# Optimization experiments

Measured on AMD Instinct MI355X. Metric: run time of the kernel, lower is better.

The kernel has to match this reference:

```python
import jax, jax.numpy as jnp
import numpy as np

B, N, C, H, W = 16, 10, 128, 48, 48

def setup_inputs() -> dict:
    key = jax.random.key(0)
    k0, k1 = jax.random.split(key, 2)
    x = jax.random.normal(k0, (B, N, C, H, W), dtype=jnp.float32)
    # trainable interpolation params, initialized to 0.5 as in the torch module
    pos_dec = jnp.full((N,), 0.5, dtype=jnp.float32)
    length_dec = jnp.full((N,), 0.5, dtype=jnp.float32)
    # 1x1 conv == channel-mixing matmul over N*C channels
    NC = N * C
    conv_w = jax.random.normal(k1, (NC, NC), dtype=jnp.float32) * (1.0 / np.sqrt(NC))
    conv_b = jnp.zeros((NC,), dtype=jnp.float32)
    return {"x": x, "pos_dec": pos_dec, "length_dec": length_dec,
            "conv_w": conv_w, "conv_b": conv_b}


def reference(x, pos_dec, length_dec, conv_w, conv_b):
    b, n, c, h, w = x.shape
    d = c * h * w
    q = x.reshape(b, n, d)          # proj_query (B,N,CHW)
    k = q                           # proj_key has the same flattened features
    # bi_interpolate with pos_int=i, length_int=1 reduces in closed form to:
    #   s0 = (1-pd)*K[i]   + pd*K[i+1]                      (key_short row)
    #   s1 = ld*((1-pd)*K[i+1] + pd*K[i+2])                 (zero-padded short mixed with key_long)
    # where indices wrap mod N (key was concatenated with itself).
    idx = jnp.arange(n)
    k1_ = k[:, (idx + 1) % n]       # (B,N,D)
    k2_ = k[:, (idx + 2) % n]
    pd = pos_dec[None, :, None]
    ld = length_dec[None, :, None]
    s0 = (1.0 - pd) * k + pd * k1_
    s1 = ld * ((1.0 - pd) * k1_ + pd * k2_)
    S = jnp.stack([s0, s1], axis=2)                 # (B,N,2,D) interpolated keys per group
    logits = jnp.einsum('bnd,bnkd->bnk', q, S)      # per-group 2-way attention scores
    attn = jax.nn.softmax(logits, axis=-1)          # softmax over the 2 searched keys
    out = jnp.einsum('bnk,bnkd->bnd', attn, S)      # (B,N,D)
    feat = out.reshape(b, n * c, h, w)
    conv = jnp.einsum('oc,bchw->bohw', conv_w, feat) + conv_b[None, :, None, None]
    return conv + x.reshape(b, n * c, h, w)
```

## Files before the change

kernel.cpp:

```cpp
#include <hip/hip_runtime.h>
#include <hip/hip_bf16.h>

#define BB 16
#define NN 10
#define CC 128
#define HWD 2304
#define DD (CC*HWD)
#define NC (NN*CC)

#define CHP 72

#define BM 256
#define BN 256
#define BK 64
#define TK (NC/BK)

typedef __bf16 bf16x8 __attribute__((ext_vector_type(8)));
typedef float  f32x4  __attribute__((ext_vector_type(4)));
typedef float  f32x16 __attribute__((ext_vector_type(16)));

#define XT_BYTES ((size_t)BB*HWD*NC*2)
#define W2_BYTES ((size_t)BB*NC*NC*2)
#define WB_BYTES ((size_t)NC*NC*2)
#define PART_FLOATS (BB*NN*CHP*3)
#define HEAD ((size_t)262144)

__device__ __forceinline__ ushort f2bf(float f) {
    __hip_bfloat16 h = __float2bfloat16(f);
    return *reinterpret_cast<ushort*>(&h);
}

__device__ __forceinline__ void gload_lds16(const ushort* g, ushort* l) {
    __builtin_amdgcn_global_load_lds(
        (const __attribute__((address_space(1))) void*)(const void*)g,
        (__attribute__((address_space(3))) void*)(void*)l,
        16, 0, 0);
}

__global__ __launch_bounds__(256) void k_trans(const float* __restrict__ x,
                                               ushort* __restrict__ xT,
                                               float* __restrict__ part) {
    __shared__ float tile[32*129];
    __shared__ float red[4][3];
    int hwt = blockIdx.x;
    int b   = blockIdx.y;
    int t = threadIdx.x;
    int hw0 = hwt*32;
    const float* xb = x + (size_t)b*NN*DD;

    int c_[4], ch_[4];
    size_t off_[4];
    #pragma unroll
    for (int i = 0; i < 4; ++i) {
        int s = i*256 + t;
        c_[i] = s >> 3; ch_[i] = s & 7;
        off_[i] = (size_t)c_[i]*HWD + hw0 + ch_[i]*4;
    }

    float4 s0[4], s1[4], s2[4], s3[4];
    #pragma unroll
    for (int i = 0; i < 4; ++i) s0[i] = *(const float4*)(xb + (size_t)0*DD + off_[i]);
    #pragma unroll
    for (int i = 0; i < 4; ++i) s1[i] = *(const float4*)(xb + (size_t)1*DD + off_[i]);
    #pragma unroll
    for (int i = 0; i < 4; ++i) s2[i] = *(const float4*)(xb + (size_t)2*DD + off_[i]);

    int w = t >> 6, l = t & 63;

    for (int n = 0; n < NN; ++n) {
        int n3 = (n + 3) % NN;
        #pragma unroll
        for (int i = 0; i < 4; ++i) s3[i] = *(const float4*)(xb + (size_t)n3*DD + off_[i]);

        float d0 = 0.f, d1 = 0.f, d2 = 0.f;
        #pragma unroll
        for (int i = 0; i < 4; ++i) {
            d0 += s0[i].x*s0[i].x + s0[i].y*s0[i].y + s0[i].z*s0[i].z + s0[i].w*s0[i].w;
            d1 += s0[i].x*s1[i].x + s0[i].y*s1[i].y + s0[i].z*s1[i].z + s0[i].w*s1[i].w;
            d2 += s0[i].x*s2[i].x + s0[i].y*s2[i].y + s0[i].z*s2[i].z + s0[i].w*s2[i].w;
        }
        for (int o = 32; o > 0; o >>= 1) {
            d0 += __shfl_down(d0, o);
            d1 += __shfl_down(d1, o);
            d2 += __shfl_down(d2, o);
        }
        if (l == 0) { red[w][0] = d0; red[w][1] = d1; red[w][2] = d2; }

        #pragma unroll
        for (int i = 0; i < 4; ++i) {
            int hwb = ch_[i]*4, cc = c_[i];
            tile[(hwb+0)*129 + cc] = s0[i].x;
            tile[(hwb+1)*129 + cc] = s0[i].y;
            tile[(hwb+2)*129 + cc] = s0[i].z;
            tile[(hwb+3)*129 + cc] = s0[i].w;
        }
        __syncthreads();

        if (t == 0) {
            float r0 = 0.f, r1 = 0.f, r2 = 0.f;
            #pragma unroll
            for (int i = 0; i < 4; ++i) { r0 += red[i][0]; r1 += red[i][1]; r2 += red[i][2]; }
            float* o = part + ((size_t)(b*NN + n)*CHP + hwt)*3;
            o[0] = r0; o[1] = r1; o[2] = r2;
        }

        int hwl = t >> 4;
        int cc0 = (t & 15) * 8;
        #pragma unroll
        for (int p = 0; p < 2; ++p) {
            int hw = p*16 + hwl;
            const float* src = &tile[hw*129 + cc0];
            union { ushort us[8]; uint4 v; } pk;
            #pragma unroll
            for (int j = 0; j < 8; ++j) pk.us[j] = f2bf(src[j]);
            ushort* dst = xT + (size_t)b*HWD*NC + (size_t)(hw0 + hw)*NC + n*CC + cc0;
            *(uint4*)dst = pk.v;
        }
        __syncthreads();
        #pragma unroll
        for (int i = 0; i < 4; ++i) { s0[i] = s1[i]; s1[i] = s2[i]; s2[i] = s3[i]; }
    }
}

__global__ void k_coef(const float* __restrict__ part,
                       const float* __restrict__ pos_dec,
                       const float* __restrict__ len_dec,
                       float* __restrict__ coef) {
    int bn = threadIdx.x;
    if (bn >= BB*NN) return;
    int n = bn % NN;
    float d0 = 0.f, d1 = 0.f, d2 = 0.f;
    const float* p = part + (size_t)bn*CHP*3;
    for (int i = 0; i < CHP; ++i) { d0 += p[i*3]; d1 += p[i*3+1]; d2 += p[i*3+2]; }
    float pd = pos_dec[n], ld = len_dec[n];
    float l0 = (1.f - pd)*d0 + pd*d1;
    float l1 = ld*((1.f - pd)*d1 + pd*d2);
    float m  = fmaxf(l0, l1);
    float e0 = expf(l0 - m), e1 = expf(l1 - m);
    float inv = 1.f/(e0 + e1);
    float a0 = e0*inv, a1 = e1*inv;
    coef[bn*3+0] = a0*(1.f - pd);
    coef[bn*3+1] = a0*pd + a1*ld*(1.f - pd);
    coef[bn*3+2] = a1*ld*pd;
}

__global__ __launch_bounds__(256) void k_w2(const float* __restrict__ w,
                                            const float* __restrict__ coef,
                                            ushort* __restrict__ w2) {
    int b = blockIdx.y;
    size_t eid = ((size_t)blockIdx.x*256 + threadIdx.x)*8;
    int o  = (int)(eid / NC);
    int mc = (int)(eid % NC);
    int m = mc >> 7, c = mc & 127;
    int m1 = (m + 9) % 10, m2 = (m + 8) % 10;
    float c0 = coef[(b*NN + m )*3 + 0];
    float c1 = coef[(b*NN + m1)*3 + 1];
    float c2 = coef[(b*NN + m2)*3 + 2];
    const float* wr = w + (size_t)o*NC;
    float4 a0 = *(const float4*)(wr + m *128 + c);
    float4 a1 = *(const float4*)(wr + m *128 + c + 4);
    float4 u0 = *(const float4*)(wr + m1*128 + c);
    float4 u1 = *(const float4*)(wr + m1*128 + c + 4);
    float4 v0 = *(const float4*)(wr + m2*128 + c);
    float4 v1 = *(const float4*)(wr + m2*128 + c + 4);
    union { ushort us[8]; uint4 v; } pk;
    pk.us[0] = f2bf(c0*a0.x + c1*u0.x + c2*v0.x);
    pk.us[1] = f2bf(c0*a0.y + c1*u0.y + c2*v0.y);
    pk.us[2] = f2bf(c0*a0.z + c1*u0.z + c2*v0.z);
    pk.us[3] = f2bf(c0*a0.w + c1*u0.w + c2*v0.w);
    pk.us[4] = f2bf(c0*a1.x + c1*u1.x + c2*v1.x);
    pk.us[5] = f2bf(c0*a1.y + c1*u1.y + c2*v1.y);
    pk.us[6] = f2bf(c0*a1.z + c1*u1.z + c2*v1.z);
    pk.us[7] = f2bf(c0*a1.w + c1*u1.w + c2*v1.w);
    *(uint4*)(w2 + (size_t)b*NC*NC + eid) = pk.v;
}

__global__ __launch_bounds__(256) void k_wconv(const float* __restrict__ w,
                                               ushort* __restrict__ wb) {
    int i = blockIdx.x*blockDim.x + threadIdx.x;
    size_t idx = (size_t)i*4;
    if (idx >= (size_t)NC*NC) return;
    float4 a = *(const float4*)(w + idx);
    ushort4 o;
    o.x = f2bf(a.x); o.y = f2bf(a.y); o.z = f2bf(a.z); o.w = f2bf(a.w);
    *(ushort4*)(wb + idx) = o;
}

__global__ __launch_bounds__(256) void k_feat(const float* __restrict__ x,
                                              const float* __restrict__ coef,
                                              ushort* __restrict__ featT) {
    __shared__ float tile[32*129];
    int hwt = blockIdx.x;
    int b   = blockIdx.y;
    int t = threadIdx.x;
    int hw0 = hwt*32;
    const float* xb = x + (size_t)b*NN*DD;

    int c_[4], ch_[4];
    size_t off_[4];
    #pragma unroll
    for (int i = 0; i < 4; ++i) {
        int s = i*256 + t;
        c_[i] = s >> 3; ch_[i] = s & 7;
        off_[i] = (size_t)c_[i]*HWD + hw0 + ch_[i]*4;
    }

    float4 s0[4], s1[4], s2[4], s3[4];
    #pragma unroll
    for (int i = 0; i < 4; ++i) s0[i] = *(const float4*)(xb + (size_t)0*DD + off_[i]);
    #pragma unroll
    for (int i = 0; i < 4; ++i) s1[i] = *(const float4*)(xb + (size_t)1*DD + off_[i]);
    #pragma unroll
    for (int i = 0; i < 4; ++i) s2[i] = *(const float4*)(xb + (size_t)2*DD + off_[i]);

    for (int n = 0; n < NN; ++n) {
        int n3 = (n + 3) % NN;
        #pragma unroll
        for (int i = 0; i < 4; ++i) s3[i] = *(const float4*)(xb + (size_t)n3*DD + off_[i]);

        int bn = b*NN + n;
        float c0 = coef[bn*3+0], c1 = coef[bn*3+1], c2 = coef[bn*3+2];

        #pragma unroll
        for (int i = 0; i < 4; ++i) {
            int hwb = ch_[i]*4, cc = c_[i];
            tile[(hwb+0)*129 + cc] = c0*s0[i].x + c1*s1[i].x + c2*s2[i].x;
            tile[(hwb+1)*129 + cc] = c0*s0[i].y + c1*s1[i].y + c2*s2[i].y;
            tile[(hwb+2)*129 + cc] = c0*s0[i].z + c1*s1[i].z + c2*s2[i].z;
            tile[(hwb+3)*129 + cc] = c0*s0[i].w + c1*s1[i].w + c2*s2[i].w;
        }
        __syncthreads();

        int hwl = t >> 4;
        int cc0 = (t & 15) * 8;
        #pragma unroll
        for (int p = 0; p < 2; ++p) {
            int hw = p*16 + hwl;
            const float* src = &tile[hw*129 + cc0];
            union { ushort us[8]; uint4 v; } pk;
            #pragma unroll
            for (int j = 0; j < 8; ++j) pk.us[j] = f2bf(src[j]);
            ushort* dst = featT + (size_t)b*HWD*NC + (size_t)(hw0 + hw)*NC + n*CC + cc0;
            *(uint4*)dst = pk.v;
        }
        __syncthreads();
        #pragma unroll
        for (int i = 0; i < 4; ++i) { s0[i] = s1[i]; s1[i] = s2[i]; s2[i] = s3[i]; }
    }
}

#define BAR()   __builtin_amdgcn_s_barrier()
#define SB()    __builtin_amdgcn_sched_barrier(0)
#define LGKM0() asm volatile("s_waitcnt lgkmcnt(0)" ::: "memory")
#define VM(N)   asm volatile("s_waitcnt vmcnt(" #N ")" ::: "memory")

__global__ __launch_bounds__(512, 2) void k_gemm(const ushort* __restrict__ Amat,
                                                 const ushort* __restrict__ Bmat,
                                                 const float* __restrict__ bias,
                                                 const float* __restrict__ x,
                                                 float* __restrict__ out,
                                                 size_t aStride) {
    __shared__ ushort L[2][4][BM*32];

    int bid = blockIdx.x;
    int wkid = (bid & 7) * 90 + (bid >> 3);
    int b   = wkid / 45;
    int r45 = wkid % 45;
    int hwt = r45 / 5;
    int ot  = r45 % 5;
    int o0 = ot*BM, hw0 = hwt*BN;

    int t = threadIdx.x;
    int l = t & 63;
    int w = t >> 6;
    int wr = w >> 2, wc = w & 3;

    const ushort* Ag = Amat + (size_t)b*aStride + (size_t)o0*NC;
    const ushort* Bg = Bmat + (size_t)b*HWD*NC + (size_t)hw0*NC;

    int r0 = t >> 2, c0 = t & 3;
    size_t g0 = (size_t)r0*NC + (size_t)((c0 ^ ((r0 >> 1) & 3)) * 8);
    size_t g1 = g0 + (size_t)128*NC;

#define STAGE(nb_, reg_, gp_) do { \
    gload_lds16((gp_) + g0, &L[nb_][reg_][t*8]); \
    gload_lds16((gp_) + g1, &L[nb_][reg_][(512 + t)*8]); } while (0)

    int fr32 = l & 31;
    int kh   = l >> 5;
    int sw   = (fr32 >> 1) & 3;
    int kcA  = ((kh)     ^ sw) << 3;
    int kcB  = ((2 | kh) ^ sw) << 3;
    int rA   = (wr*128 + fr32)*32;
    int rB   = (wc*64  + fr32)*32;

    f32x16 acc[4][2] = {};
    bf16x8 af[8], bf0, bf1;

    STAGE(0, 0, Ag);
    STAGE(0, 2, Bg);
    STAGE(0, 1, Ag + 32);
    STAGE(0, 3, Bg + 32);
    VM(4);
    BAR(); SB();

#define MFMA8(accn_) do { \
    _Pragma("unroll") \
    for (int mt = 0; mt < 4; ++mt) { \
        acc[mt][accn_] = __builtin_amdgcn_mfma_f32_32x32x16_bf16(af[mt*2+0], bf0, acc[mt][accn_], 0, 0, 0); \
        acc[mt][accn_] = __builtin_amdgcn_mfma_f32_32x32x16_bf16(af[mt*2+1], bf1, acc[mt][accn_], 0, 0, 0); \
    } } while (0)

    for (int kt = 0; kt < TK - 1; ++kt) {
        int buf = kt & 1, nbuf = buf ^ 1;
        const ushort* A0 = &L[buf][0][0];
        const ushort* A1 = &L[buf][1][0];
        const ushort* B0 = &L[buf][2][0];
        const ushort* B1 = &L[buf][3][0];
        const ushort* Agk = Ag + (size_t)(kt + 1)*BK;
        const ushort* Bgk = Bg + (size_t)(kt + 1)*BK;

        #pragma unroll
        for (int mt = 0; mt < 4; ++mt) {
            af[mt*2+0] = *(const bf16x8*)&A0[rA + mt*1024 + kcA];
            af[mt*2+1] = *(const bf16x8*)&A0[rA + mt*1024 + kcB];
        }
        bf0 = *(const bf16x8*)&B0[rB + kcA];
        bf1 = *(const bf16x8*)&B0[rB + kcB];
        STAGE(nbuf, 0, Agk);
        SB(); BAR(); LGKM0(); SB();
        __builtin_amdgcn_s_setprio(1);
        MFMA8(0);
        __builtin_amdgcn_s_setprio(0);
        SB(); BAR(); SB();

        bf0 = *(const bf16x8*)&B0[rB + 1024 + kcA];
        bf1 = *(const bf16x8*)&B0[rB + 1024 + kcB];
        STAGE(nbuf, 2, Bgk);
        SB(); BAR(); LGKM0(); SB();
        __builtin_amdgcn_s_setprio(1);
        MFMA8(1);
        __builtin_amdgcn_s_setprio(0);
        SB(); VM(4); BAR(); SB();

        #pragma unroll
        for (int mt = 0; mt < 4; ++mt) {
            af[mt*2+0] = *(const bf16x8*)&A1[rA + mt*1024 + kcA];
            af[mt*2+1] = *(const bf16x8*)&A1[rA + mt*1024 + kcB];
        }
        bf0 = *(const bf16x8*)&B1[rB + kcA];
        bf1 = *(const bf16x8*)&B1[rB + kcB];
        STAGE(nbuf, 1, Agk + 32);
        SB(); BAR(); LGKM0(); SB();
        __builtin_amdgcn_s_setprio(1);
        MFMA8(0);
        __builtin_amdgcn_s_setprio(0);
        SB(); BAR(); SB();

        bf0 = *(const bf16x8*)&B1[rB + 1024 + kcA];
        bf1 = *(const bf16x8*)&B1[rB + 1024 + kcB];
        STAGE(nbuf, 3, Bgk + 32);
        SB(); BAR(); LGKM0(); SB();
        __builtin_amdgcn_s_setprio(1);
        MFMA8(1);
        __builtin_amdgcn_s_setprio(0);
        SB(); VM(4); BAR(); SB();
    }

    {
        const int buf = (TK - 1) & 1;
        const ushort* A0 = &L[buf][0][0];
        const ushort* A1 = &L[buf][1][0];
        const ushort* B0 = &L[buf][2][0];
        const ushort* B1 = &L[buf][3][0];

        #pragma unroll
        for (int mt = 0; mt < 4; ++mt) {
            af[mt*2+0] = *(const bf16x8*)&A0[rA + mt*1024 + kcA];
            af[mt*2+1] = *(const bf16x8*)&A0[rA + mt*1024 + kcB];
        }
        bf0 = *(const bf16x8*)&B0[rB + kcA];
        bf1 = *(const bf16x8*)&B0[rB + kcB];
        MFMA8(0);
        bf0 = *(const bf16x8*)&B0[rB + 1024 + kcA];
        bf1 = *(const bf16x8*)&B0[rB + 1024 + kcB];
        MFMA8(1);
        VM(0);
        BAR(); SB();
        #pragma unroll
        for (int mt = 0; mt < 4; ++mt) {
            af[mt*2+0] = *(const bf16x8*)&A1[rA + mt*1024 + kcA];
            af[mt*2+1] = *(const bf16x8*)&A1[rA + mt*1024 + kcB];
        }
        bf0 = *(const bf16x8*)&B1[rB + kcA];
        bf1 = *(const bf16x8*)&B1[rB + kcB];
        MFMA8(0);
        bf0 = *(const bf16x8*)&B1[rB + 1024 + kcA];
        bf1 = *(const bf16x8*)&B1[rB + 1024 + kcB];
        MFMA8(1);
    }
#undef MFMA8
#undef STAGE

    #pragma unroll
    for (int mt = 0; mt < 4; ++mt) {
        #pragma unroll
        for (int nt = 0; nt < 2; ++nt) {
            int col = hw0 + wc*64 + nt*32 + fr32;
            #pragma unroll
            for (int reg = 0; reg < 16; ++reg) {
                int ro = o0 + wr*128 + mt*32 + (reg & 3) + 8*(reg >> 2) + 4*kh;
                size_t idx = (size_t)b*NC*HWD + (size_t)ro*HWD + col;
                out[idx] = acc[mt][nt][reg] + bias[ro] + x[idx];
            }
        }
    }
}

extern "C" void kernel_launch(void* const* d_in, const int* in_sizes, int n_in,
                              void* d_out, int out_size, void* d_ws, size_t ws_size,
                              hipStream_t stream) {
    const float* x       = (const float*)d_in[0];
    const float* pos_dec = (const float*)d_in[1];
    const float* len_dec = (const float*)d_in[2];
    const float* conv_w  = (const float*)d_in[3];
    const float* conv_b  = (const float*)d_in[4];
    float* out = (float*)d_out;

    char* ws = (char*)d_ws;
    float*  part = (float*)ws;
    float*  coef = part + PART_FLOATS;
    ushort* xT   = (ushort*)(ws + HEAD);

    k_trans<<<dim3(CHP, BB), 256, 0, stream>>>(x, xT, part);
    k_coef <<<dim3(1), 256, 0, stream>>>(part, pos_dec, len_dec, coef);

    if (ws_size >= HEAD + XT_BYTES + W2_BYTES) {
        ushort* w2 = (ushort*)(ws + HEAD + XT_BYTES);
        k_w2  <<<dim3(800, BB), 256, 0, stream>>>(conv_w, coef, w2);
        k_gemm<<<dim3(720), 512, 0, stream>>>(w2, xT, conv_b, x, out, (size_t)NC*NC);
    } else {
        ushort* wb = (ushort*)(ws + HEAD + XT_BYTES);
        k_wconv<<<dim3(1600), 256, 0, stream>>>(conv_w, wb);
        k_feat <<<dim3(CHP, BB), 256, 0, stream>>>(x, coef, xT);
        k_gemm <<<dim3(720), 512, 0, stream>>>(wb, xT, conv_b, x, out, (size_t)0);
    }
}
```

Baseline: 272.4 us.

## Rework GEMM to smaller tiles with triple-buffered LDS pipeline and nontemporal epilogue

The GEMM kernel drops its 256x256x64 tile with a hand-scheduled double-buffered four-phase loop and uses a 128x256x32 tile with a three-slot LDS ring, prefetching two K-steps ahead and syncing once per step. The grid doubles to 1440 blocks and launch bounds ask for 4 blocks per CU, aiming at higher occupancy and latency hiding. The epilogue switches to nontemporal loads and stores for the residual and output. Smaller M tiles cut data reuse per block and raise global/LDS traffic per FLOP, and the setprio and fine-grained barrier scheduling are gone.

```diff
diff --git a/kernel.cpp b/kernel.cpp
--- a/kernel.cpp
+++ b/kernel.cpp
@@ -10,9 +10,9 @@
 
 #define CHP 72
 
-#define BM 256
+#define BM 128
 #define BN 256
-#define BK 64
+#define BK 32
 #define TK (NC/BK)
 
 typedef __bf16 bf16x8 __attribute__((ext_vector_type(8)));
@@ -21,7 +21,6 @@
 
 #define XT_BYTES ((size_t)BB*HWD*NC*2)
 #define W2_BYTES ((size_t)BB*NC*NC*2)
-#define WB_BYTES ((size_t)NC*NC*2)
 #define PART_FLOATS (BB*NN*CHP*3)
 #define HEAD ((size_t)262144)
 
@@ -251,23 +250,23 @@
 
 #define BAR()   __builtin_amdgcn_s_barrier()
 #define SB()    __builtin_amdgcn_sched_barrier(0)
-#define LGKM0() asm volatile("s_waitcnt lgkmcnt(0)" ::: "memory")
 #define VM(N)   asm volatile("s_waitcnt vmcnt(" #N ")" ::: "memory")
 
-__global__ __launch_bounds__(512, 2) void k_gemm(const ushort* __restrict__ Amat,
+__global__ __launch_bounds__(512, 4) void k_gemm(const ushort* __restrict__ Amat,
                                                  const ushort* __restrict__ Bmat,
                                                  const float* __restrict__ bias,
                                                  const float* __restrict__ x,
                                                  float* __restrict__ out,
                                                  size_t aStride) {
-    __shared__ ushort L[2][4][BM*32];
+    __shared__ ushort LA[3][BM*BK];
+    __shared__ ushort LB[3][BN*BK];
 
     int bid = blockIdx.x;
-    int wkid = (bid & 7) * 90 + (bid >> 3);
-    int b   = wkid / 45;
-    int r45 = wkid % 45;
-    int hwt = r45 / 5;
-    int ot  = r45 % 5;
+    int wkid = (bid & 7) * 180 + (bid >> 3);
+    int b    = wkid / 90;
+    int rem  = wkid % 90;
+    int hwt  = rem / 10;
+    int ot   = rem % 10;
     int o0 = ot*BM, hw0 = hwt*BN;
 
     int t = threadIdx.x;
@@ -278,140 +277,86 @@
     const ushort* Ag = Amat + (size_t)b*aStride + (size_t)o0*NC;
     const ushort* Bg = Bmat + (size_t)b*HWD*NC + (size_t)hw0*NC;
 
-    int r0 = t >> 2, c0 = t & 3;
-    size_t g0 = (size_t)r0*NC + (size_t)((c0 ^ ((r0 >> 1) & 3)) * 8);
-    size_t g1 = g0 + (size_t)128*NC;
-
-#define STAGE(nb_, reg_, gp_) do { \
-    gload_lds16((gp_) + g0, &L[nb_][reg_][t*8]); \
-    gload_lds16((gp_) + g1, &L[nb_][reg_][(512 + t)*8]); } while (0)
+    int sr = t >> 2, sc = t & 3;
+    size_t gA  = (size_t)sr*NC + (size_t)((sc ^ ((sr >> 1) & 3)) * 8);
+    size_t gB0 = gA;
+    size_t gB1 = gA + (size_t)128*NC;
+
+#define STAGE(sl_, kt_) do { \
+    size_t ko_ = (size_t)(kt_)*BK; \
+    gload_lds16(Ag + gA  + ko_, &LA[sl_][t*8]); \
+    gload_lds16(Bg + gB0 + ko_, &LB[sl_][t*8]); \
+    gload_lds16(Bg + gB1 + ko_, &LB[sl_][(512 + t)*8]); } while (0)
 
     int fr32 = l & 31;
     int kh   = l >> 5;
     int sw   = (fr32 >> 1) & 3;
-    int kcA  = ((kh)     ^ sw) << 3;
-    int kcB  = ((2 | kh) ^ sw) << 3;
-    int rA   = (wr*128 + fr32)*32;
-    int rB   = (wc*64  + fr32)*32;
-
-    f32x16 acc[4][2] = {};
-    bf16x8 af[8], bf0, bf1;
-
-    STAGE(0, 0, Ag);
-    STAGE(0, 2, Bg);
-    STAGE(0, 1, Ag + 32);
-    STAGE(0, 3, Bg + 32);
-    VM(4);
+    int kc0  = ((kh)     ^ sw) << 3;
+    int kc1  = ((2 | kh) ^ sw) << 3;
+    int rA   = (wr*64 + fr32)*BK;
+    int rB   = (wc*64 + fr32)*BK;
+
+    f32x16 acc[2][2] = {};
+    bf16x8 a0f, a1f, b0f, b1f;
+
+#define COMPUTE(sl_) do { \
+    const ushort* As_ = &LA[sl_][0]; \
+    const ushort* Bs_ = &LB[sl_][0]; \
+     \
+    a0f = *(const bf16x8*)&As_[rA + kc0]; \
+    a1f = *(const bf16x8*)&As_[rA + 1024 + kc0]; \
+    b0f = *(const bf16x8*)&Bs_[rB + kc0]; \
+    b1f = *(const bf16x8*)&Bs_[rB + 1024 + kc0]; \
+    acc[0][0] = __builtin_amdgcn_mfma_f32_32x32x16_bf16(a0f, b0f, acc[0][0], 0, 0, 0); \
+    acc[0][1] = __builtin_amdgcn_mfma_f32_32x32x16_bf16(a0f, b1f, acc[0][1], 0, 0, 0); \
+    acc[1][0] = __builtin_amdgcn_mfma_f32_32x32x16_bf16(a1f, b0f, acc[1][0], 0, 0, 0); \
+    acc[1][1] = __builtin_amdgcn_mfma_f32_32x32x16_bf16(a1f, b1f, acc[1][1], 0, 0, 0); \
+     \
+    a0f = *(const bf16x8*)&As_[rA + kc1]; \
+    a1f = *(const bf16x8*)&As_[rA + 1024 + kc1]; \
+    b0f = *(const bf16x8*)&Bs_[rB + kc1]; \
+    b1f = *(const bf16x8*)&Bs_[rB + 1024 + kc1]; \
+    acc[0][0] = __builtin_amdgcn_mfma_f32_32x32x16_bf16(a0f, b0f, acc[0][0], 0, 0, 0); \
+    acc[0][1] = __builtin_amdgcn_mfma_f32_32x32x16_bf16(a0f, b1f, acc[0][1], 0, 0, 0); \
+    acc[1][0] = __builtin_amdgcn_mfma_f32_32x32x16_bf16(a1f, b0f, acc[1][0], 0, 0, 0); \
+    acc[1][1] = __builtin_amdgcn_mfma_f32_32x32x16_bf16(a1f, b1f, acc[1][1], 0, 0, 0); \
+} while (0)
+
+    STAGE(0, 0);
+    STAGE(1, 1);
+    VM(3);
     BAR(); SB();
 
-#define MFMA8(accn_) do { \
-    _Pragma("unroll") \
-    for (int mt = 0; mt < 4; ++mt) { \
-        acc[mt][accn_] = __builtin_amdgcn_mfma_f32_32x32x16_bf16(af[mt*2+0], bf0, acc[mt][accn_], 0, 0, 0); \
-        acc[mt][accn_] = __builtin_amdgcn_mfma_f32_32x32x16_bf16(af[mt*2+1], bf1, acc[mt][accn_], 0, 0, 0); \
-    } } while (0)
-
-    for (int kt = 0; kt < TK - 1; ++kt) {
-        int buf = kt & 1, nbuf = buf ^ 1;
-        const ushort* A0 = &L[buf][0][0];
-        const ushort* A1 = &L[buf][1][0];
-        const ushort* B0 = &L[buf][2][0];
-        const ushort* B1 = &L[buf][3][0];
-        const ushort* Agk = Ag + (size_t)(kt + 1)*BK;
-        const ushort* Bgk = Bg + (size_t)(kt + 1)*BK;
-
-        #pragma unroll
-        for (int mt = 0; mt < 4; ++mt) {
-            af[mt*2+0] = *(const bf16x8*)&A0[rA + mt*1024 + kcA];
-            af[mt*2+1] = *(const bf16x8*)&A0[rA + mt*1024 + kcB];
-        }
-        bf0 = *(const bf16x8*)&B0[rB + kcA];
-        bf1 = *(const bf16x8*)&B0[rB + kcB];
-        STAGE(nbuf, 0, Agk);
-        SB(); BAR(); LGKM0(); SB();
-        __builtin_amdgcn_s_setprio(1);
-        MFMA8(0);
-        __builtin_amdgcn_s_setprio(0);
-        SB(); BAR(); SB();
-
-        bf0 = *(const bf16x8*)&B0[rB + 1024 + kcA];
-        bf1 = *(const bf16x8*)&B0[rB + 1024 + kcB];
-        STAGE(nbuf, 2, Bgk);
-        SB(); BAR(); LGKM0(); SB();
-        __builtin_amdgcn_s_setprio(1);
-        MFMA8(1);
-        __builtin_amdgcn_s_setprio(0);
-        SB(); VM(4); BAR(); SB();
-
-        #pragma unroll
-        for (int mt = 0; mt < 4; ++mt) {
-            af[mt*2+0] = *(const bf16x8*)&A1[rA + mt*1024 + kcA];
-            af[mt*2+1] = *(const bf16x8*)&A1[rA + mt*1024 + kcB];
-        }
-        bf0 = *(const bf16x8*)&B1[rB + kcA];
-        bf1 = *(const bf16x8*)&B1[rB + kcB];
-        STAGE(nbuf, 1, Agk + 32);
-        SB(); BAR(); LGKM0(); SB();
-        __builtin_amdgcn_s_setprio(1);
-        MFMA8(0);
-        __builtin_amdgcn_s_setprio(0);
-        SB(); BAR(); SB();
-
-        bf0 = *(const bf16x8*)&B1[rB + 1024 + kcA];
-        bf1 = *(const bf16x8*)&B1[rB + 1024 + kcB];
-        STAGE(nbuf, 3, Bgk + 32);
-        SB(); BAR(); LGKM0(); SB();
-        __builtin_amdgcn_s_setprio(1);
-        MFMA8(1);
-        __builtin_amdgcn_s_setprio(0);
-        SB(); VM(4); BAR(); SB();
-    }
-
-    {
-        const int buf = (TK - 1) & 1;
-        const ushort* A0 = &L[buf][0][0];
-        const ushort* A1 = &L[buf][1][0];
-        const ushort* B0 = &L[buf][2][0];
-        const ushort* B1 = &L[buf][3][0];
-
-        #pragma unroll
-        for (int mt = 0; mt < 4; ++mt) {
-            af[mt*2+0] = *(const bf16x8*)&A0[rA + mt*1024 + kcA];
-            af[mt*2+1] = *(const bf16x8*)&A0[rA + mt*1024 + kcB];
-        }
-        bf0 = *(const bf16x8*)&B0[rB + kcA];
-        bf1 = *(const bf16x8*)&B0[rB + kcB];
-        MFMA8(0);
-        bf0 = *(const bf16x8*)&B0[rB + 1024 + kcA];
-        bf1 = *(const bf16x8*)&B0[rB + 1024 + kcB];
-        MFMA8(1);
-        VM(0);
+    int cur = 0, stg = 2;
+    for (int kt = 0; kt < TK - 2; ++kt) {
+        STAGE(stg, kt + 2);
+        SB();
+        COMPUTE(cur);
+        VM(3);
         BAR(); SB();
-        #pragma unroll
-        for (int mt = 0; mt < 4; ++mt) {
-            af[mt*2+0] = *(const bf16x8*)&A1[rA + mt*1024 + kcA];
-            af[mt*2+1] = *(const bf16x8*)&A1[rA + mt*1024 + kcB];
-        }
-        bf0 = *(const bf16x8*)&B1[rB + kcA];
-        bf1 = *(const bf16x8*)&B1[rB + kcB];
-        MFMA8(0);
-        bf0 = *(const bf16x8*)&B1[rB + 1024 + kcA];
-        bf1 = *(const bf16x8*)&B1[rB + 1024 + kcB];
-        MFMA8(1);
-    }
-#undef MFMA8
+        cur = (cur == 2) ? 0 : cur + 1;
+        stg = (stg == 2) ? 0 : stg + 1;
+    }
+    COMPUTE(cur);
+    VM(0);
+    BAR(); SB();
+    cur = (cur == 2) ? 0 : cur + 1;
+    COMPUTE(cur);
+
+#undef COMPUTE
 #undef STAGE
 
     #pragma unroll
-    for (int mt = 0; mt < 4; ++mt) {
+    for (int mt = 0; mt < 2; ++mt) {
         #pragma unroll
         for (int nt = 0; nt < 2; ++nt) {
             int col = hw0 + wc*64 + nt*32 + fr32;
             #pragma unroll
             for (int reg = 0; reg < 16; ++reg) {
-                int ro = o0 + wr*128 + mt*32 + (reg & 3) + 8*(reg >> 2) + 4*kh;
+                int ro = o0 + wr*64 + mt*32 + (reg & 3) + 8*(reg >> 2) + 4*kh;
                 size_t idx = (size_t)b*NC*HWD + (size_t)ro*HWD + col;
-                out[idx] = acc[mt][nt][reg] + bias[ro] + x[idx];
+                float xv = __builtin_nontemporal_load(&x[idx]);
+                __builtin_nontemporal_store(acc[mt][nt][reg] + bias[ro] + xv, &out[idx]);
             }
         }
     }
@@ -438,11 +383,11 @@
     if (ws_size >= HEAD + XT_BYTES + W2_BYTES) {
         ushort* w2 = (ushort*)(ws + HEAD + XT_BYTES);
         k_w2  <<<dim3(800, BB), 256, 0, stream>>>(conv_w, coef, w2);
-        k_gemm<<<dim3(720), 512, 0, stream>>>(w2, xT, conv_b, x, out, (size_t)NC*NC);
+        k_gemm<<<dim3(1440), 512, 0, stream>>>(w2, xT, conv_b, x, out, (size_t)NC*NC);
     } else {
         ushort* wb = (ushort*)(ws + HEAD + XT_BYTES);
         k_wconv<<<dim3(1600), 256, 0, stream>>>(conv_w, wb);
         k_feat <<<dim3(CHP, BB), 256, 0, stream>>>(x, coef, xT);
-        k_gemm <<<dim3(720), 512, 0, stream>>>(wb, xT, conv_b, x, out, (size_t)0);
-    }
-}
+        k_gemm <<<dim3(1440), 512, 0, stream>>>(wb, xT, conv_b, x, out, (size_t)0);
+    }
+}
```

Result: slower. 280.4 us (+3.0%).

## Collapse GEMM k-loop into two phases per iteration with fewer barriers

Applied to the files above, without the earlier changes.

The bf16 MFMA GEMM main loop used to run four sub-phases per k-tile. Each one loaded fragments, issued one LDS stage, then hit barriers and lgkmcnt waits, with s_setprio raised around the MFMA burst. It now has two phases per iteration. Each phase issues two async global-to-LDS stages, loads all A and B fragments for the 32-wide k-slice, runs 16 MFMAs, then waits on vmcnt and hits one barrier. This cuts barrier and wait overhead and leaves the compiler free to interleave LDS reads with MFMAs. The trade-off is more live fragment registers, the loss of explicit priority boosting, and less control over how LDS reads overlap with the in-flight global loads.

```diff
diff --git a/kernel.cpp b/kernel.cpp
--- a/kernel.cpp
+++ b/kernel.cpp
@@ -21,7 +21,6 @@
 
 #define XT_BYTES ((size_t)BB*HWD*NC*2)
 #define W2_BYTES ((size_t)BB*NC*NC*2)
-#define WB_BYTES ((size_t)NC*NC*2)
 #define PART_FLOATS (BB*NN*CHP*3)
 #define HEAD ((size_t)262144)
 
@@ -251,7 +250,6 @@
 
 #define BAR()   __builtin_amdgcn_s_barrier()
 #define SB()    __builtin_amdgcn_sched_barrier(0)
-#define LGKM0() asm volatile("s_waitcnt lgkmcnt(0)" ::: "memory")
 #define VM(N)   asm volatile("s_waitcnt vmcnt(" #N ")" ::: "memory")
 
 __global__ __launch_bounds__(512, 2) void k_gemm(const ushort* __restrict__ Amat,
@@ -295,21 +293,32 @@
     int rB   = (wc*64  + fr32)*32;
 
     f32x16 acc[4][2] = {};
-    bf16x8 af[8], bf0, bf1;
+
+#define COMP(Ar_, Br_) do { \
+    bf16x8 a_[8], b0_, b1_, b2_, b3_; \
+    _Pragma("unroll") \
+    for (int mt = 0; mt < 4; ++mt) { \
+        a_[mt*2+0] = *(const bf16x8*)&(Ar_)[rA + mt*1024 + kcA]; \
+        a_[mt*2+1] = *(const bf16x8*)&(Ar_)[rA + mt*1024 + kcB]; \
+    } \
+    b0_ = *(const bf16x8*)&(Br_)[rB + kcA]; \
+    b1_ = *(const bf16x8*)&(Br_)[rB + kcB]; \
+    b2_ = *(const bf16x8*)&(Br_)[rB + 1024 + kcA]; \
+    b3_ = *(const bf16x8*)&(Br_)[rB + 1024 + kcB]; \
+    _Pragma("unroll") \
+    for (int mt = 0; mt < 4; ++mt) { \
+        acc[mt][0] = __builtin_amdgcn_mfma_f32_32x32x16_bf16(a_[mt*2+0], b0_, acc[mt][0], 0, 0, 0); \
+        acc[mt][0] = __builtin_amdgcn_mfma_f32_32x32x16_bf16(a_[mt*2+1], b1_, acc[mt][0], 0, 0, 0); \
+        acc[mt][1] = __builtin_amdgcn_mfma_f32_32x32x16_bf16(a_[mt*2+0], b2_, acc[mt][1], 0, 0, 0); \
+        acc[mt][1] = __builtin_amdgcn_mfma_f32_32x32x16_bf16(a_[mt*2+1], b3_, acc[mt][1], 0, 0, 0); \
+    } } while (0)
 
     STAGE(0, 0, Ag);
     STAGE(0, 2, Bg);
     STAGE(0, 1, Ag + 32);
     STAGE(0, 3, Bg + 32);
     VM(4);
-    BAR(); SB();
-
-#define MFMA8(accn_) do { \
-    _Pragma("unroll") \
-    for (int mt = 0; mt < 4; ++mt) { \
-        acc[mt][accn_] = __builtin_amdgcn_mfma_f32_32x32x16_bf16(af[mt*2+0], bf0, acc[mt][accn_], 0, 0, 0); \
-        acc[mt][accn_] = __builtin_amdgcn_mfma_f32_32x32x16_bf16(af[mt*2+1], bf1, acc[mt][accn_], 0, 0, 0); \
-    } } while (0)
+    BAR();
 
     for (int kt = 0; kt < TK - 1; ++kt) {
         int buf = kt & 1, nbuf = buf ^ 1;
@@ -320,86 +329,29 @@
         const ushort* Agk = Ag + (size_t)(kt + 1)*BK;
         const ushort* Bgk = Bg + (size_t)(kt + 1)*BK;
 
-        #pragma unroll
-        for (int mt = 0; mt < 4; ++mt) {
-            af[mt*2+0] = *(const bf16x8*)&A0[rA + mt*1024 + kcA];
-            af[mt*2+1] = *(const bf16x8*)&A0[rA + mt*1024 + kcB];
-        }
-        bf0 = *(const bf16x8*)&B0[rB + kcA];
-        bf1 = *(const bf16x8*)&B0[rB + kcB];
         STAGE(nbuf, 0, Agk);
-        SB(); BAR(); LGKM0(); SB();
-        __builtin_amdgcn_s_setprio(1);
-        MFMA8(0);
-        __builtin_amdgcn_s_setprio(0);
-        SB(); BAR(); SB();
-
-        bf0 = *(const bf16x8*)&B0[rB + 1024 + kcA];
-        bf1 = *(const bf16x8*)&B0[rB + 1024 + kcB];
         STAGE(nbuf, 2, Bgk);
-        SB(); BAR(); LGKM0(); SB();
-        __builtin_amdgcn_s_setprio(1);
-        MFMA8(1);
-        __builtin_amdgcn_s_setprio(0);
-        SB(); VM(4); BAR(); SB();
-
-        #pragma unroll
-        for (int mt = 0; mt < 4; ++mt) {
-            af[mt*2+0] = *(const bf16x8*)&A1[rA + mt*1024 + kcA];
-            af[mt*2+1] = *(const bf16x8*)&A1[rA + mt*1024 + kcB];
-        }
-        bf0 = *(const bf16x8*)&B1[rB + kcA];
-        bf1 = *(const bf16x8*)&B1[rB + kcB];
+        SB();
+        COMP(A0, B0);
+        VM(4);
+        BAR();
+
         STAGE(nbuf, 1, Agk + 32);
-        SB(); BAR(); LGKM0(); SB();
-        __builtin_amdgcn_s_setprio(1);
-        MFMA8(0);
-        __builtin_amdgcn_s_setprio(0);
-        SB(); BAR(); SB();
-
-        bf0 = *(const bf16x8*)&B1[rB + 1024 + kcA];
-        bf1 = *(const bf16x8*)&B1[rB + 1024 + kcB];
         STAGE(nbuf, 3, Bgk + 32);
-        SB(); BAR(); LGKM0(); SB();
-        __builtin_amdgcn_s_setprio(1);
-        MFMA8(1);
-        __builtin_amdgcn_s_setprio(0);
-        SB(); VM(4); BAR(); SB();
+        SB();
+        COMP(A1, B1);
+        VM(4);
+        BAR();
     }
 
     {
         const int buf = (TK - 1) & 1;
-        const ushort* A0 = &L[buf][0][0];
-        const ushort* A1 = &L[buf][1][0];
-        const ushort* B0 = &L[buf][2][0];
-        const ushort* B1 = &L[buf][3][0];
-
-        #pragma unroll
-        for (int mt = 0; mt < 4; ++mt) {
-            af[mt*2+0] = *(const bf16x8*)&A0[rA + mt*1024 + kcA];
-            af[mt*2+1] = *(const bf16x8*)&A0[rA + mt*1024 + kcB];
-        }
-        bf0 = *(const bf16x8*)&B0[rB + kcA];
-        bf1 = *(const bf16x8*)&B0[rB + kcB];
-        MFMA8(0);
-        bf0 = *(const bf16x8*)&B0[rB + 1024 + kcA];
-        bf1 = *(const bf16x8*)&B0[rB + 1024 + kcB];
-        MFMA8(1);
+        COMP((&L[buf][0][0]), (&L[buf][2][0]));
         VM(0);
-        BAR(); SB();
-        #pragma unroll
-        for (int mt = 0; mt < 4; ++mt) {
-            af[mt*2+0] = *(const bf16x8*)&A1[rA + mt*1024 + kcA];
-            af[mt*2+1] = *(const bf16x8*)&A1[rA + mt*1024 + kcB];
-        }
-        bf0 = *(const bf16x8*)&B1[rB + kcA];
-        bf1 = *(const bf16x8*)&B1[rB + kcB];
-        MFMA8(0);
-        bf0 = *(const bf16x8*)&B1[rB + 1024 + kcA];
-        bf1 = *(const bf16x8*)&B1[rB + 1024 + kcB];
-        MFMA8(1);
-    }
-#undef MFMA8
+        BAR();
+        COMP((&L[buf][1][0]), (&L[buf][3][0]));
+    }
+#undef COMP
 #undef STAGE
 
     #pragma unroll
```

Result: no change. 268.4 us, median of 2 (-1.4%).
